# Optimization experiments

Hardware: AMD Instinct MI355X
Metric: run time of the kernel (lower is better)

## Reference

```python
import jax, jax.numpy as jnp
import numpy as np

NUM_TRACKS = [5313, 1643, 128, 0]
MAX_TRACKS = max(NUM_TRACKS)
EMBED_DIM = 1536
LN_EPS = 1e-5


def setup_inputs() -> dict:
    key = jax.random.key(0)
    ks = jax.random.split(key, 8)
    B, S, D = 4, 896, EMBED_DIM
    inp = {
        "x": jax.random.normal(ks[0], (B, S, D), dtype=jnp.float32),
        "head_idx": jax.random.randint(ks[1], (B,), 0, 4, dtype=jnp.int64) if jax.config.jax_enable_x64 else jax.random.randint(ks[1], (B,), 0, 4).astype(jnp.int32),
    }
    for i, n in enumerate([5313, 1643, 128]):
        inp[f"gamma{i}"] = jnp.ones((D,), jnp.float32)
        inp[f"beta{i}"] = jnp.zeros((D,), jnp.float32)
        inp[f"W{i}"] = jax.random.normal(ks[2 + i], (n, D), dtype=jnp.float32) * 0.02
        inp[f"b{i}"] = jnp.zeros((n,), jnp.float32)
    return inp


def _linear_head(x, gamma, beta, W, b):
    # LayerNormFP32 -> Linear -> softplus, cast back to orig dtype
    orig_dtype = x.dtype
    xf = x.astype(jnp.float32)
    mu = jnp.mean(xf, axis=-1, keepdims=True)
    var = jnp.var(xf, axis=-1, keepdims=True)  # biased, as torch LayerNorm
    xn = (xf - mu) * jax.lax.rsqrt(var + LN_EPS) * gamma + beta
    h = jax.nn.softplus(jnp.einsum("bsd,td->bst", xn, W) + b)
    return h.astype(orig_dtype)


def reference(x, head_idx, gamma0, beta0, W0, b0,
              gamma1, beta1, W1, b1, gamma2, beta2, W2, b2):
    params = [(gamma0, beta0, W0, b0),
              (gamma1, beta1, W1, b1),
              (gamma2, beta2, W2, b2),
              None]  # ZeroHead
    B, S, _ = x.shape
    logits = jnp.zeros((B, S, MAX_TRACKS), dtype=x.dtype)
    for i, p in enumerate(params):
        if p is None:
            padded = jnp.zeros((B, S, MAX_TRACKS), dtype=x.dtype)
        else:
            h = _linear_head(x, *p)  # [B, S, n_i]
            pad = MAX_TRACKS - h.shape[-1]
            padded = jnp.pad(h, ((0, 0), (0, 0), (0, pad))) if pad > 0 else h
        mask = (head_idx == i)[:, None, None]
        logits = jnp.where(mask, padded, logits)
    return logits
```

## Files before the change

kernel.cpp:

```cpp
#include <hip/hip_runtime.h>
#include <hip/hip_bf16.h>

#define EMBED 1536
#define SEQ   896
#define NOUT  5313

#define N0 5313
#define N1 1643
#define N2 128
#define W0OFF 0
#define W1OFF 5376
#define W2OFF 7040
#define PTOT  7168

#define LN_BLOCKS 1792
#define WC_BLOCKS 5376
#define ZF_BLOCKS 3584
#define GEMM_MAXBLOCKS 1176

typedef __attribute__((ext_vector_type(8))) short bf16x8;
typedef __attribute__((ext_vector_type(4))) float f32x4;

__device__ __forceinline__ void gload_lds16(const void* g, void* l) {
    __builtin_amdgcn_global_load_lds(
        (const __attribute__((address_space(1))) void*)g,
        (__attribute__((address_space(3))) void*)l, 16, 0, 0);
}

__device__ __forceinline__ int tiles_of(int h) {
    return (h == 0) ? 42 : (h == 1) ? 13 : (h == 2) ? 1 : 0;
}
__device__ __forceinline__ int nrows_of(int h) {
    return (h == 0) ? N0 : (h == 1) ? N1 : (h == 2) ? N2 : 0;
}

__global__ __launch_bounds__(256) void prep_kernel(
    const float* __restrict__ x, const int* __restrict__ head_idx,
    const float* __restrict__ g0, const float* __restrict__ be0,
    const float* __restrict__ g1, const float* __restrict__ be1,
    const float* __restrict__ g2, const float* __restrict__ be2,
    const float* __restrict__ W0, const float* __restrict__ W1,
    const float* __restrict__ W2,
    __hip_bfloat16* __restrict__ xn, __hip_bfloat16* __restrict__ wpad,
    float* __restrict__ out)
{
    const int tid = threadIdx.x;

    if (blockIdx.x < LN_BLOCKS) {
        const int half = tid >> 7;
        const int lt   = tid & 127;
        const int row  = blockIdx.x * 2 + half;
        const int b    = row / SEQ;
        const int h    = head_idx[b];
        if (h == 3) return;

        const float* gamma = (h == 1) ? g1 : (h == 2) ? g2 : g0;
        const float* beta  = (h == 1) ? be1 : (h == 2) ? be2 : be0;
        const float* xr = x + (size_t)row * EMBED;

        float4 v[3];
        float sum = 0.f, sq = 0.f;
#pragma unroll
        for (int i = 0; i < 3; ++i) {
            v[i] = ((const float4*)xr)[lt + i * 128];
            sum += v[i].x + v[i].y + v[i].z + v[i].w;
            sq  += v[i].x * v[i].x + v[i].y * v[i].y + v[i].z * v[i].z + v[i].w * v[i].w;
        }
#pragma unroll
        for (int off = 32; off > 0; off >>= 1) {
            sum += __shfl_down(sum, off);
            sq  += __shfl_down(sq, off);
        }
        __shared__ float s_sum[4], s_sq[4];
        const int wave = tid >> 6, lane = tid & 63;
        if (lane == 0) { s_sum[wave] = sum; s_sq[wave] = sq; }
        __syncthreads();
        const int wb = half << 1;
        const float mu  = (s_sum[wb] + s_sum[wb + 1]) * (1.f / EMBED);
        const float var = (s_sq[wb] + s_sq[wb + 1]) * (1.f / EMBED) - mu * mu;
        const float rs  = rsqrtf(var + 1e-5f);

        __hip_bfloat16* xo = xn + (size_t)row * EMBED;
#pragma unroll
        for (int i = 0; i < 3; ++i) {
            const int idx = lt + i * 128;
            float4 gv = ((const float4*)gamma)[idx];
            float4 bv = ((const float4*)beta)[idx];
            union { __hip_bfloat16 h4[4]; short4 s4; } u;
            u.h4[0] = __float2bfloat16((v[i].x - mu) * rs * gv.x + bv.x);
            u.h4[1] = __float2bfloat16((v[i].y - mu) * rs * gv.y + bv.y);
            u.h4[2] = __float2bfloat16((v[i].z - mu) * rs * gv.z + bv.z);
            u.h4[3] = __float2bfloat16((v[i].w - mu) * rs * gv.w + bv.w);
            ((short4*)xo)[idx] = u.s4;
        }
    } else if (blockIdx.x < LN_BLOCKS + WC_BLOCKS) {
        const int gid = (blockIdx.x - LN_BLOCKS) * 256 + tid;
        const int r = gid / 192;
        const int c = (gid - r * 192) * 8;
        const int region = (r < W1OFF) ? 0 : (r < W2OFF) ? 1 : 2;
        const int h0 = head_idx[0], h1 = head_idx[1];
        const int h2 = head_idx[2], h3 = head_idx[3];
        if (region != h0 && region != h1 && region != h2 && region != h3)
            return;
        const float* src = nullptr;
        if (region == 0)      { if (r < N0) src = W0 + (size_t)r * EMBED; }
        else if (region == 1) { int rr = r - W1OFF; if (rr < N1) src = W1 + (size_t)rr * EMBED; }
        else                  { int rr = r - W2OFF; if (rr < N2) src = W2 + (size_t)rr * EMBED; }
        union { __hip_bfloat16 h8[8]; int4 v4; } u;
        if (src) {
            float4 a = ((const float4*)(src + c))[0];
            float4 b = ((const float4*)(src + c))[1];
            u.h8[0] = __float2bfloat16(a.x); u.h8[1] = __float2bfloat16(a.y);
            u.h8[2] = __float2bfloat16(a.z); u.h8[3] = __float2bfloat16(a.w);
            u.h8[4] = __float2bfloat16(b.x); u.h8[5] = __float2bfloat16(b.y);
            u.h8[6] = __float2bfloat16(b.z); u.h8[7] = __float2bfloat16(b.w);
        } else {
            u.v4 = make_int4(0, 0, 0, 0);
        }
        *(int4*)(wpad + (size_t)r * EMBED + c) = u.v4;
    } else {
        const int row = blockIdx.x - (LN_BLOCKS + WC_BLOCKS);
        const int b = row / SEQ;
        const int h = head_idx[b];
        const int n = nrows_of(h);
        if (n >= NOUT) return;
        float* o = out + (size_t)row * NOUT;
        const int pre0 = (4 - (int)(((size_t)row * NOUT + n) & 3)) & 3;
        const int pre_end = min(n + pre0, NOUT);
        for (int c = n + tid; c < pre_end; c += 256) o[c] = 0.f;
        const int nvec = (NOUT - pre_end) >> 2;
        const float4 z = make_float4(0.f, 0.f, 0.f, 0.f);
        float4* ov = (float4*)(o + pre_end);
        for (int i = tid; i < nvec; i += 256) ov[i] = z;
        for (int c = pre_end + (nvec << 2) + tid; c < NOUT; c += 256) o[c] = 0.f;
    }
}

__global__ __launch_bounds__(256, 2) void head_gemm(
    const __hip_bfloat16* __restrict__ xn,
    const __hip_bfloat16* __restrict__ wpad,
    const float* __restrict__ b0, const float* __restrict__ b1,
    const float* __restrict__ b2,
    const int* __restrict__ head_idx,
    float* __restrict__ out)
{
    const int h0 = head_idx[0], h1 = head_idx[1];
    const int h2 = head_idx[2], h3 = head_idx[3];
    const int t0 = tiles_of(h0) * 7, t1 = tiles_of(h1) * 7;
    const int t2 = tiles_of(h2) * 7, t3 = tiles_of(h3) * 7;

    int rem = blockIdx.x, b;
    if (rem < t0)                { b = 0; }
    else if (rem < t0 + t1)      { b = 1; rem -= t0; }
    else if (rem < t0 + t1 + t2) { b = 2; rem -= t0 + t1; }
    else if (rem < t0 + t1 + t2 + t3) { b = 3; rem -= t0 + t1 + t2; }
    else return;

    const int h = (b == 0) ? h0 : (b == 1) ? h1 : (b == 2) ? h2 : h3;
    const int ntc = tiles_of(h);
    const int mt = rem / ntc;
    const int nt = rem - mt * ntc;
    const int nrows = nrows_of(h);
    const int wbase = (h == 0) ? W0OFF : (h == 1) ? W1OFF : W2OFF;

    const int tid = threadIdx.x;
    const int col0 = nt * 128;
    float* outb = out + ((size_t)b * SEQ + (size_t)mt * 128) * NOUT;

    __shared__ __hip_bfloat16 As[128 * 64];
    __shared__ __hip_bfloat16 Bs[128 * 64];
    const __hip_bfloat16* Ab = xn + ((size_t)b * SEQ + (size_t)mt * 128) * EMBED;
    const __hip_bfloat16* Bb = wpad + (size_t)(wbase + col0) * EMBED;

    const int wave = tid >> 6, lane = tid & 63;
    const int wm = wave >> 1, wn = wave & 1;
    const int fm = lane & 15, quad = lane >> 4;
    const int fsw = fm & 7;

    f32x4 acc[4][4] = {};

    for (int kt = 0; kt < EMBED / 64; ++kt) {
        const int k0 = kt * 64;
        __syncthreads();
#pragma unroll
        for (int i = 0; i < 4; ++i) {
            const int c = tid + i * 256;
            const int arow = c >> 3;
            const int kc = (c & 7) ^ (arow & 7);
            gload_lds16(Ab + (size_t)arow * EMBED + k0 + kc * 8, As + c * 8);
        }
#pragma unroll
        for (int i = 0; i < 4; ++i) {
            const int c = tid + i * 256;
            const int brow = c >> 3;
            const int kc = (c & 7) ^ (brow & 7);
            gload_lds16(Bb + (size_t)brow * EMBED + k0 + kc * 8, Bs + c * 8);
        }
        __syncthreads();
#pragma unroll
        for (int ks = 0; ks < 2; ++ks) {
            bf16x8 af[4], bfr[4];
#pragma unroll
            for (int i = 0; i < 4; ++i)
                af[i] = *(const bf16x8*)&As[(wm * 64 + i * 16 + fm) * 64 +
                                            (((ks << 2) + quad) ^ fsw) * 8];
#pragma unroll
            for (int j = 0; j < 4; ++j)
                bfr[j] = *(const bf16x8*)&Bs[(wn * 64 + j * 16 + fm) * 64 +
                                             (((ks << 2) + quad) ^ fsw) * 8];
#pragma unroll
            for (int i = 0; i < 4; ++i)
#pragma unroll
                for (int j = 0; j < 4; ++j)
                    acc[i][j] = __builtin_amdgcn_mfma_f32_16x16x32_bf16(
                        af[i], bfr[j], acc[i][j], 0, 0, 0);
        }
    }

    const float* bias = (h == 1) ? b1 : (h == 2) ? b2 : b0;
#pragma unroll
    for (int j = 0; j < 4; ++j) {
        const int lcol = col0 + wn * 64 + j * 16 + fm;
        const bool valid = lcol < nrows;
        const float bv = valid ? bias[lcol] : 0.f;
#pragma unroll
        for (int i = 0; i < 4; ++i) {
            const int rbase = wm * 64 + i * 16 + quad * 4;
#pragma unroll
            for (int r = 0; r < 4; ++r) {
                const float v = acc[i][j][r] + bv;
                const float sp = fmaxf(v, 0.f) + __logf(1.f + __expf(-fabsf(v)));
                if (valid) outb[(size_t)(rbase + r) * NOUT + lcol] = sp;
            }
        }
    }
}

extern "C" void kernel_launch(void* const* d_in, const int* in_sizes, int n_in,
                              void* d_out, int out_size, void* d_ws, size_t ws_size,
                              hipStream_t stream) {
    const float* x   = (const float*)d_in[0];
    const int* hidx  = (const int*)d_in[1];
    const float* g0  = (const float*)d_in[2];
    const float* be0 = (const float*)d_in[3];
    const float* W0  = (const float*)d_in[4];
    const float* b0  = (const float*)d_in[5];
    const float* g1  = (const float*)d_in[6];
    const float* be1 = (const float*)d_in[7];
    const float* W1  = (const float*)d_in[8];
    const float* b1  = (const float*)d_in[9];
    const float* g2  = (const float*)d_in[10];
    const float* be2 = (const float*)d_in[11];
    const float* W2  = (const float*)d_in[12];
    const float* b2  = (const float*)d_in[13];
    float* out = (float*)d_out;

    const size_t XN_BYTES = (size_t)4 * SEQ * EMBED * 2;
    __hip_bfloat16* xn   = (__hip_bfloat16*)d_ws;
    __hip_bfloat16* wpad = (__hip_bfloat16*)((char*)d_ws + XN_BYTES);

    prep_kernel<<<LN_BLOCKS + WC_BLOCKS + ZF_BLOCKS, 256, 0, stream>>>(
        x, hidx, g0, be0, g1, be1, g2, be2, W0, W1, W2, xn, wpad, out);
    head_gemm<<<GEMM_MAXBLOCKS, 256, 0, stream>>>(xn, wpad, b0, b1, b2, hidx, out);
}
```

Baseline: 179.6 us.

## Halve GEMM M-tile to 64 rows and move zero-fill into spare GEMM blocks

The GEMM tile changes from 128x128 to 64x128. This doubles the number of work blocks, which should help fill the GPU when few heads are active, and lowers per-block register and LDS use. The zero-fill of padded output columns moves out of the prep kernel into the leftover blocks of the GEMM grid, so those stores run alongside the matmul instead of before it. The cost is less A/B reuse per block, which means more weight traffic from L2, and the zero-fill is now spread over however many blocks are spare.

```diff
diff --git a/kernel.cpp b/kernel.cpp
--- a/kernel.cpp
+++ b/kernel.cpp
@@ -15,8 +15,8 @@
 
 #define LN_BLOCKS 1792
 #define WC_BLOCKS 5376
-#define ZF_BLOCKS 3584
-#define GEMM_MAXBLOCKS 1176
+#define MT64 14
+#define GEMM_GRID 2352
 
 typedef __attribute__((ext_vector_type(8))) short bf16x8;
 typedef __attribute__((ext_vector_type(4))) float f32x4;
@@ -41,8 +41,7 @@
     const float* __restrict__ g2, const float* __restrict__ be2,
     const float* __restrict__ W0, const float* __restrict__ W1,
     const float* __restrict__ W2,
-    __hip_bfloat16* __restrict__ xn, __hip_bfloat16* __restrict__ wpad,
-    float* __restrict__ out)
+    __hip_bfloat16* __restrict__ xn, __hip_bfloat16* __restrict__ wpad)
 {
     const int tid = threadIdx.x;
 
@@ -93,7 +92,7 @@
             u.h4[3] = __float2bfloat16((v[i].w - mu) * rs * gv.w + bv.w);
             ((short4*)xo)[idx] = u.s4;
         }
-    } else if (blockIdx.x < LN_BLOCKS + WC_BLOCKS) {
+    } else {
         const int gid = (blockIdx.x - LN_BLOCKS) * 256 + tid;
         const int r = gid / 192;
         const int c = (gid - r * 192) * 8;
@@ -118,21 +117,6 @@
             u.v4 = make_int4(0, 0, 0, 0);
         }
         *(int4*)(wpad + (size_t)r * EMBED + c) = u.v4;
-    } else {
-        const int row = blockIdx.x - (LN_BLOCKS + WC_BLOCKS);
-        const int b = row / SEQ;
-        const int h = head_idx[b];
-        const int n = nrows_of(h);
-        if (n >= NOUT) return;
-        float* o = out + (size_t)row * NOUT;
-        const int pre0 = (4 - (int)(((size_t)row * NOUT + n) & 3)) & 3;
-        const int pre_end = min(n + pre0, NOUT);
-        for (int c = n + tid; c < pre_end; c += 256) o[c] = 0.f;
-        const int nvec = (NOUT - pre_end) >> 2;
-        const float4 z = make_float4(0.f, 0.f, 0.f, 0.f);
-        float4* ov = (float4*)(o + pre_end);
-        for (int i = tid; i < nvec; i += 256) ov[i] = z;
-        for (int c = pre_end + (nvec << 2) + tid; c < NOUT; c += 256) o[c] = 0.f;
     }
 }
 
@@ -146,15 +130,37 @@
 {
     const int h0 = head_idx[0], h1 = head_idx[1];
     const int h2 = head_idx[2], h3 = head_idx[3];
-    const int t0 = tiles_of(h0) * 7, t1 = tiles_of(h1) * 7;
-    const int t2 = tiles_of(h2) * 7, t3 = tiles_of(h3) * 7;
+    const int t0 = tiles_of(h0) * MT64, t1 = tiles_of(h1) * MT64;
+    const int t2 = tiles_of(h2) * MT64, t3 = tiles_of(h3) * MT64;
+    const int R = t0 + t1 + t2 + t3;
+    const int tid = threadIdx.x;
+
+    if ((int)blockIdx.x >= R) {
+        const int j = blockIdx.x - R;
+        const int ZB = GEMM_GRID - R;
+        for (int row = j; row < 4 * SEQ; row += ZB) {
+            const int b = row / SEQ;
+            const int h = (b == 0) ? h0 : (b == 1) ? h1 : (b == 2) ? h2 : h3;
+            const int n = nrows_of(h);
+            if (n >= NOUT) continue;
+            float* o = out + (size_t)row * NOUT;
+            const int pre0 = (4 - (int)(((size_t)row * NOUT + n) & 3)) & 3;
+            const int pre_end = min(n + pre0, NOUT);
+            for (int c = n + tid; c < pre_end; c += 256) o[c] = 0.f;
+            const int nvec = (NOUT - pre_end) >> 2;
+            const float4 z = make_float4(0.f, 0.f, 0.f, 0.f);
+            float4* ov = (float4*)(o + pre_end);
+            for (int i = tid; i < nvec; i += 256) ov[i] = z;
+            for (int c = pre_end + (nvec << 2) + tid; c < NOUT; c += 256) o[c] = 0.f;
+        }
+        return;
+    }
 
     int rem = blockIdx.x, b;
-    if (rem < t0)                { b = 0; }
-    else if (rem < t0 + t1)      { b = 1; rem -= t0; }
+    if (rem < t0)           { b = 0; }
+    else if (rem < t0 + t1) { b = 1; rem -= t0; }
     else if (rem < t0 + t1 + t2) { b = 2; rem -= t0 + t1; }
-    else if (rem < t0 + t1 + t2 + t3) { b = 3; rem -= t0 + t1 + t2; }
-    else return;
+    else                    { b = 3; rem -= t0 + t1 + t2; }
 
     const int h = (b == 0) ? h0 : (b == 1) ? h1 : (b == 2) ? h2 : h3;
     const int ntc = tiles_of(h);
@@ -163,13 +169,12 @@
     const int nrows = nrows_of(h);
     const int wbase = (h == 0) ? W0OFF : (h == 1) ? W1OFF : W2OFF;
 
-    const int tid = threadIdx.x;
     const int col0 = nt * 128;
-    float* outb = out + ((size_t)b * SEQ + (size_t)mt * 128) * NOUT;
-
-    __shared__ __hip_bfloat16 As[128 * 64];
+    float* outb = out + ((size_t)b * SEQ + (size_t)mt * 64) * NOUT;
+
+    __shared__ __hip_bfloat16 As[64 * 64];
     __shared__ __hip_bfloat16 Bs[128 * 64];
-    const __hip_bfloat16* Ab = xn + ((size_t)b * SEQ + (size_t)mt * 128) * EMBED;
+    const __hip_bfloat16* Ab = xn + ((size_t)b * SEQ + (size_t)mt * 64) * EMBED;
     const __hip_bfloat16* Bb = wpad + (size_t)(wbase + col0) * EMBED;
 
     const int wave = tid >> 6, lane = tid & 63;
@@ -177,13 +182,13 @@
     const int fm = lane & 15, quad = lane >> 4;
     const int fsw = fm & 7;
 
-    f32x4 acc[4][4] = {};
+    f32x4 acc[2][4] = {};
 
     for (int kt = 0; kt < EMBED / 64; ++kt) {
         const int k0 = kt * 64;
         __syncthreads();
 #pragma unroll
-        for (int i = 0; i < 4; ++i) {
+        for (int i = 0; i < 2; ++i) {
             const int c = tid + i * 256;
             const int arow = c >> 3;
             const int kc = (c & 7) ^ (arow & 7);
@@ -199,17 +204,17 @@
         __syncthreads();
 #pragma unroll
         for (int ks = 0; ks < 2; ++ks) {
-            bf16x8 af[4], bfr[4];
-#pragma unroll
-            for (int i = 0; i < 4; ++i)
-                af[i] = *(const bf16x8*)&As[(wm * 64 + i * 16 + fm) * 64 +
+            bf16x8 af[2], bfr[4];
+#pragma unroll
+            for (int i = 0; i < 2; ++i)
+                af[i] = *(const bf16x8*)&As[(wm * 32 + i * 16 + fm) * 64 +
                                             (((ks << 2) + quad) ^ fsw) * 8];
 #pragma unroll
             for (int j = 0; j < 4; ++j)
                 bfr[j] = *(const bf16x8*)&Bs[(wn * 64 + j * 16 + fm) * 64 +
                                              (((ks << 2) + quad) ^ fsw) * 8];
 #pragma unroll
-            for (int i = 0; i < 4; ++i)
+            for (int i = 0; i < 2; ++i)
 #pragma unroll
                 for (int j = 0; j < 4; ++j)
                     acc[i][j] = __builtin_amdgcn_mfma_f32_16x16x32_bf16(
@@ -224,8 +229,8 @@
         const bool valid = lcol < nrows;
         const float bv = valid ? bias[lcol] : 0.f;
 #pragma unroll
-        for (int i = 0; i < 4; ++i) {
-            const int rbase = wm * 64 + i * 16 + quad * 4;
+        for (int i = 0; i < 2; ++i) {
+            const int rbase = wm * 32 + i * 16 + quad * 4;
 #pragma unroll
             for (int r = 0; r < 4; ++r) {
                 const float v = acc[i][j][r] + bv;
@@ -259,7 +264,7 @@
     __hip_bfloat16* xn   = (__hip_bfloat16*)d_ws;
     __hip_bfloat16* wpad = (__hip_bfloat16*)((char*)d_ws + XN_BYTES);
 
-    prep_kernel<<<LN_BLOCKS + WC_BLOCKS + ZF_BLOCKS, 256, 0, stream>>>(
-        x, hidx, g0, be0, g1, be1, g2, be2, W0, W1, W2, xn, wpad, out);
-    head_gemm<<<GEMM_MAXBLOCKS, 256, 0, stream>>>(xn, wpad, b0, b1, b2, hidx, out);
-}
+    prep_kernel<<<LN_BLOCKS + WC_BLOCKS, 256, 0, stream>>>(
+        x, hidx, g0, be0, g1, be1, g2, be2, W0, W1, W2, xn, wpad);
+    head_gemm<<<GEMM_GRID, 256, 0, stream>>>(xn, wpad, b0, b1, b2, hidx, out);
+}
```

Measured after the change: 175.5 us. -2.3%, faster.
